# Optimization experiments

Hardware: AMD Instinct MI355X
Metric: run time of the kernel (lower is better)

Reference implementation:

```python
import jax, jax.numpy as jnp
import numpy as np

DIST = 200.0
BBOX_SP = 24
N_COARSE = 64
N_BOXES = 10
SAMPLES_ALL = N_COARSE + 2 * N_BOXES  # 84
FR_POS = 10
FR_DIR = 4
NSEM = 50
WID = 256
MERGES = [(39, 41), (27, 26), (28, 26), (29, 26), (30, 26), (31, 26), (9, 8), (35, 13)]


def posenc(x, L):
    f = 2.0 ** jnp.arange(L, dtype=x.dtype)
    xb = x[..., None, :] * f[:, None]                      # [..., L, 3]
    enc = jnp.concatenate([jnp.sin(xb), jnp.cos(xb)], -1)  # [..., L, 6]
    return jnp.concatenate([x, enc.reshape(x.shape[:-1] + (-1,))], -1)


def sample_pdf(bins, weights, n):
    # deterministic inverse-CDF sampling (det=True), bins [B,N,M], weights [B,N,M-1]
    pdf = weights / jnp.sum(weights, -1, keepdims=True)
    cdf = jnp.cumsum(pdf, -1)
    cdf = jnp.concatenate([jnp.zeros_like(cdf[..., :1]), cdf], -1)   # [B,N,M]
    B, N, M = cdf.shape
    u = jnp.linspace(0.0, 1.0, n, dtype=bins.dtype)
    cdf_f = cdf.reshape(B * N, M)
    bins_f = bins.reshape(B * N, M)
    u_f = jnp.broadcast_to(u, (B * N, n))
    inds = jax.vmap(lambda c, uu: jnp.searchsorted(c, uu, side='right'))(cdf_f, u_f)
    below = jnp.clip(inds - 1, 0, M - 1)
    above = jnp.clip(inds, 0, M - 1)
    cdf_b = jnp.take_along_axis(cdf_f, below, 1)
    cdf_a = jnp.take_along_axis(cdf_f, above, 1)
    bin_b = jnp.take_along_axis(bins_f, below, 1)
    bin_a = jnp.take_along_axis(bins_f, above, 1)
    denom = jnp.where(cdf_a - cdf_b < 1e-5, 1.0, cdf_a - cdf_b)
    t = (u_f - cdf_b) / denom
    return (bin_b + t * (bin_a - bin_b)).reshape(B, N, n)


def setup_inputs() -> dict:
    key = jax.random.key(0)
    ks = jax.random.split(key, 16)
    B, N = 1, 2048
    rays_o = jax.random.normal(ks[0], (B, N, 3)) * 2.0
    rays_d = jax.random.normal(ks[1], (B, N, 3))
    rays = jnp.concatenate([rays_o, rays_d], -1)
    near = jax.random.uniform(ks[2], (B, N, N_BOXES), minval=5.0, maxval=150.0)
    far = near + jax.random.uniform(ks[3], (B, N, N_BOXES), minval=5.0, maxval=60.0)
    inst = jax.random.randint(ks[4], (B, N, N_BOXES), 0, 20).astype(jnp.float32)
    label = jax.random.randint(ks[5], (B, N, N_BOXES), 1, NSEM).astype(jnp.float32)
    intersection = jnp.stack([near, far, inst, label], -1)  # [B,N,10,4]
    bg_noise = jax.random.uniform(ks[6], (B, N, SAMPLES_ALL))

    def lin(k, fi, fo):
        return jax.random.normal(k, (fi, fo)) / np.sqrt(fi)

    d_x = 3 + 6 * FR_POS  # 63
    d_d = 3 + 6 * FR_DIR  # 27
    params = dict(
        w_in=lin(ks[7], d_x, WID), b_in=jnp.zeros((WID,)),
        w_h=jax.random.normal(ks[8], (6, WID, WID)) / np.sqrt(WID), b_h=jnp.zeros((6, WID)),
        w_skip=lin(ks[9], WID + d_x, WID), b_skip=jnp.zeros((WID,)),
        w_sigma=lin(ks[10], WID, 1), b_sigma=jnp.zeros((1,)),
        w_feat=lin(ks[11], WID, WID), b_feat=jnp.zeros((WID,)),
        w_rgb1=lin(ks[12], WID + d_d, 128), b_rgb1=jnp.zeros((128,)),
        w_rgb2=lin(ks[13], 128, 3), b_rgb2=jnp.zeros((3,)),
        w_sem=lin(ks[14], WID, NSEM), b_sem=jnp.zeros((NSEM,)),
    )
    out = {'rays': rays, 'intersection': intersection, 'bg_noise': bg_noise}
    out.update(params)
    return out


def reference(rays, intersection, bg_noise, w_in, b_in, w_h, b_h, w_skip, b_skip,
              w_sigma, b_sigma, w_feat, b_feat, w_rgb1, b_rgb1, w_rgb2, b_rgb2,
              w_sem, b_sem):
    B, N, _ = rays.shape
    rays_o, rays_d = rays[..., :3], rays[..., 3:6]
    scale = jnp.linalg.norm(rays_d, axis=-1)  # [B,N]

    # --- ray sampling inside boxes + uniform-PDF resampling ---
    near, far = intersection[..., 0], intersection[..., 1]  # [B,N,10]
    t = jnp.linspace(0.0, 1.0, BBOX_SP)
    z_box = near[..., None] + (far - near)[..., None] * t       # [B,N,10,24]
    z_bound = jnp.concatenate([z_box[..., 0] - 1e-5, z_box[..., -1] + 1e-5], axis=2)  # [B,N,20]
    zf = jnp.sort(z_box.reshape(B, N, -1), axis=2)              # [B,N,240]
    z = sample_pdf(zf, jnp.ones_like(zf[..., 1:]), N_COARSE)    # [B,N,64]
    z = jnp.concatenate([z, z_bound], axis=2)                   # [B,N,84]
    z = jnp.where(z < 0.0, DIST + 20.0 * bg_noise, z)
    z = jnp.sort(z, axis=2)

    # --- NeRF MLP on sample points ---
    xyz = (rays_o[:, :, None] + rays_d[:, :, None] * z[..., None] / scale[..., None, None]) / DIST
    dirs = rays_d / scale[..., None]
    x_enc = posenc(xyz, FR_POS)                                 # [B,N,S,63]
    h = jax.nn.relu(x_enc @ w_in + b_in)
    for i in range(3):
        h = jax.nn.relu(h @ w_h[i] + b_h[i])
    h = jax.nn.relu(jnp.concatenate([h, x_enc], -1) @ w_skip + b_skip)
    for i in range(3, 6):
        h = jax.nn.relu(h @ w_h[i] + b_h[i])
    sigma = (h @ w_sigma + b_sigma)[..., 0]                     # [B,N,S]
    sem = h @ w_sem + b_sem                                     # [B,N,S,50]
    feat = h @ w_feat + b_feat
    d_enc = posenc(dirs, FR_DIR)                                # [B,N,27]
    d_enc = jnp.broadcast_to(d_enc[:, :, None, :], feat.shape[:-1] + (d_enc.shape[-1],))
    hr = jax.nn.relu(jnp.concatenate([feat, d_enc], -1) @ w_rgb1 + b_rgb1)
    rgb = hr @ w_rgb2 + b_rgb2                                  # [B,N,S,3]

    # --- semantic one-hot scatter + boundary masks (no-grad region) ---
    zs = jax.lax.stop_gradient(z)
    nearb = intersection[:, :, None, :, 0]                      # [B,N,1,10]
    farb = intersection[:, :, None, :, 1]
    inside = (zs[..., None] > nearb) & (zs[..., None] < farb)   # [B,N,S,10]
    d1 = zs[..., None] - farb
    d2 = nearb - zs[..., None]
    mask_bound = jnp.any(((d1 > 0) & (d1 < 1e-3)) | ((d2 > 0) & (d2 < 1e-3)), axis=-1)
    labels = intersection[..., 3].astype(jnp.int32)             # [B,N,10]
    oh_box = jax.nn.one_hot(labels, NSEM)                       # [B,N,10,50]
    one_hot = jnp.max(inside[..., None].astype(jnp.float32) * oh_box[:, :, None, :, :], axis=3)
    s0 = one_hot.sum(-1)
    mask_bbox = (zs < DIST) & (s0 == 0.0)
    mask_bg = (zs > DIST) & (s0 == 0.0)
    one_hot = one_hot.at[..., 0].set(jnp.where(mask_bbox, 1.0, one_hot[..., 0]))
    one_hot = one_hot.at[..., 23].set(jnp.where(mask_bg, 1.0, one_hot[..., 23]))
    for src, dst in MERGES:  # training-mode class merging (box/car/park/gate)
        one_hot = one_hot.at[..., dst].set(jnp.maximum(one_hot[..., dst], one_hot[..., src]))
        one_hot = one_hot.at[..., src].set(0.0)
    one_hot = jax.lax.stop_gradient(one_hot)

    # zero density outside boxes and at box boundaries
    sigma = jnp.where(mask_bbox | mask_bound, 0.0, sigma)

    # --- volumetric compositing (raw2outputs_semantic_joint) ---
    z_true = z / scale[..., None]
    dists = jnp.concatenate([z_true[..., 1:] - z_true[..., :-1],
                             jnp.full_like(z_true[..., :1], 1e10)], -1) * scale[..., None]
    alpha = 1.0 - jnp.exp(-jax.nn.relu(sigma) * dists)
    trans = jnp.cumprod(jnp.concatenate([jnp.ones_like(alpha[..., :1]),
                                         1.0 - alpha + 1e-10], -1)[..., :-1], -1)
    w = alpha * trans                                           # [B,N,S]
    rgb_map = jnp.einsum('bns,bnsc->bnc', w, jax.nn.sigmoid(rgb))
    depth = jnp.sum(w * z_true, -1)
    acc = jnp.sum(w, -1)
    sem_map = jnp.einsum('bns,bnsc->bnc', w, sem)
    return jnp.concatenate([rgb_map, depth[..., None], acc[..., None], sem_map], -1)  # [B,N,55]
```

## Files before the change

kernel.cpp:

```cpp
#include <hip/hip_runtime.h>

typedef _Float16 half8 __attribute__((ext_vector_type(8)));
typedef float f32x4 __attribute__((ext_vector_type(4)));

#define NRAYS 2048
#define SAMP 84
#define NPTS (NRAYS*SAMP)
#define SEMSTR 52

#define WT0_OFF   0
#define WTH_OFF   16384
#define WTS_OFF   409600
#define WTHD_OFF  491520
#define WTR1_OFF  573440
#define WTR2_OFF  610304
#define WT_TOTAL  612352
#define NBIAS     2512

#define OFF_WT    ((size_t)0)
#define OFF_BIAS  ((size_t)1224704)
#define OFF_Z     (OFF_BIAS + (size_t)NBIAS*4)
#define OFF_SCALE (OFF_Z + (size_t)NPTS*4)
#define OFF_SIGMA (OFF_SCALE + (size_t)NRAYS*4)
#define OFF_RGB   (OFF_SIGMA + (size_t)NPTS*4)
#define OFF_SEM   (OFF_RGB + (size_t)NPTS*12)

__global__ __launch_bounds__(256) void prep_kernel(
    const float* __restrict__ w_in,  const float* __restrict__ w_h,
    const float* __restrict__ w_skip,const float* __restrict__ w_sigma,
    const float* __restrict__ w_feat,const float* __restrict__ w_rgb1,
    const float* __restrict__ w_rgb2,const float* __restrict__ w_sem,
    const float* __restrict__ b_in,  const float* __restrict__ b_h,
    const float* __restrict__ b_skip,const float* __restrict__ b_sigma,
    const float* __restrict__ b_feat,const float* __restrict__ b_rgb1,
    const float* __restrict__ b_rgb2,const float* __restrict__ b_sem,
    _Float16* __restrict__ wt, float* __restrict__ bias)
{
  int idx = blockIdx.x*256 + threadIdx.x;
  if (idx < WT_TOTAL) {
    float v; int n, k, l, h, q;
    if (idx < WTH_OFF) {
      int r = idx; int F = r >> 10; int rem = r & 1023; int kt = rem >> 9; q = rem & 511;
      l = q >> 3; h = q & 7;
      n = F*16 + (l&15); k = kt*32 + (l>>4)*8 + h;
      v = (k < 63) ? w_in[k*256 + n] : 0.f;
    } else if (idx < WTS_OFF) {
      int r = idx - WTH_OFF; int i = r >> 16; int r2 = r & 65535;
      int F = r2 >> 12; int kt = (r2 >> 9) & 7; q = r2 & 511;
      l = q >> 3; h = q & 7;
      n = F*16 + (l&15); k = kt*32 + (l>>4)*8 + h;
      v = w_h[(i<<16) + (k<<8) + n];
    } else if (idx < WTHD_OFF) {
      int r = idx - WTS_OFF; int F = r / 5120; int rem = r % 5120; int kt = rem >> 9; q = rem & 511;
      l = q >> 3; h = q & 7;
      n = F*16 + (l&15); k = kt*32 + (l>>4)*8 + h;
      v = (k < 319) ? w_skip[k*256 + n] : 0.f;
    } else if (idx < WTR1_OFF) {
      int r = idx - WTHD_OFF; int F = r >> 12; int kt = (r >> 9) & 7; q = r & 511;
      l = q >> 3; h = q & 7;
      n = F*16 + (l&15); k = kt*32 + (l>>4)*8 + h;
      v = (n < 256) ? w_feat[(k<<8) + n]
        : (n < 306) ? w_sem[k*50 + (n-256)]
        : (n == 306)? w_sigma[k] : 0.f;
    } else if (idx < WTR2_OFF) {
      int r = idx - WTR1_OFF; int F = r / 4608; int rem = r % 4608; int kt = rem >> 9; q = rem & 511;
      l = q >> 3; h = q & 7;
      n = F*16 + (l&15); k = kt*32 + (l>>4)*8 + h;
      v = (k < 283) ? w_rgb1[k*128 + n] : 0.f;
    } else {
      int r = idx - WTR2_OFF; int kt = r >> 9; q = r & 511;
      l = q >> 3; h = q & 7;
      n = (l&15); k = kt*32 + (l>>4)*8 + h;
      v = (n < 3) ? w_rgb2[k*3 + n] : 0.f;
    }
    wt[idx] = (_Float16)v;
  } else if (idx < WT_TOTAL + NBIAS) {
    int j = idx - WT_TOTAL; float v;
    if (j < 2048) {
      int i = j >> 8, c = j & 255;
      v = (i==0) ? b_in[c] : (i<4) ? b_h[(i-1)*256+c]
        : (i==4) ? b_skip[c] : b_h[(i-2)*256+c];
    } else if (j < 2368) {
      int c = j - 2048;
      v = (c<256) ? b_feat[c] : (c<306) ? b_sem[c-256]
        : (c==306) ? b_sigma[0] : 0.f;
    } else if (j < 2496) v = b_rgb1[j-2368];
    else { int c = j-2496; v = (c<3) ? b_rgb2[c] : 0.f; }
    bias[j] = v;
  }
}

__global__ __launch_bounds__(256) void sample_kernel(
    const float* __restrict__ rays, const float* __restrict__ inter,
    const float* __restrict__ noise, float* __restrict__ zbuf,
    float* __restrict__ scaleb)
{
  __shared__ float sv[240], ss[240], z2[84];
  const int ray = blockIdx.x, t = threadIdx.x;
  const float* bx = inter + (size_t)ray*40;
  if (t < 240) {
    int b = t/24, j = t%24;
    float nr = bx[b*4], fr = bx[b*4+1];
    float tj = (j==23) ? 1.f : (float)j * (1.f/23.f);
    sv[t] = nr + (fr-nr)*tj;
  }
  __syncthreads();
  if (t < 240) {
    float v = sv[t]; int r = 0;
    for (int i = 0; i < 240; ++i) { float vi = sv[i]; r += (vi < v) || (vi == v && i < t); }
    ss[r] = v;
  }
  __syncthreads();
  if (t < 64) {
    float z;
    if (t == 63) z = ss[239];
    else { int num = t*239; int k = num/63; float f = (float)(num - k*63)*(1.f/63.f);
           z = ss[k] + f*(ss[k+1]-ss[k]); }
    z2[t] = z;
  } else if (t < 84) {
    int b = t - 64;
    z2[t] = (b < 10) ? (bx[b*4] - 1e-5f) : (bx[(b-10)*4+1] + 1e-5f);
  }
  __syncthreads();
  if (t < 84) { float z = z2[t]; if (z < 0.f) z = 200.f + 20.f*noise[(size_t)ray*84 + t]; z2[t] = z; }
  __syncthreads();
  if (t < 84) {
    float v = z2[t]; int r = 0;
    for (int i = 0; i < 84; ++i) { float vi = z2[i]; r += (vi < v) || (vi == v && i < t); }
    zbuf[(size_t)ray*84 + r] = v;
  }
  if (t == 0) {
    float dx = rays[ray*6+3], dy = rays[ray*6+4], dz = rays[ray*6+5];
    scaleb[ray] = sqrtf(dx*dx + dy*dy + dz*dz);
  }
}

#define LDS_TOTAL 81920

__device__ __forceinline__ uint32_t laddr(int m, int k) {
  return (uint32_t)(m*640) + (uint32_t)((((k>>3)^(m&7))<<4) + ((k&7)<<1));
}
struct __attribute__((aligned(8))) H4 { _Float16 h[4]; };

__device__ __forceinline__ float xenc_val(int j, float x0, float x1, float x2) {
  if (j >= 63) return 0.f;
  if (j < 3) return j==0?x0:(j==1?x1:x2);
  int q = j-3, lf = q/6, r = q%6, ci = r%3;
  float xc = (ci==0)?x0:((ci==1)?x1:x2);
  float arg = xc * (float)(1<<lf);
  return (r<3) ? sinf(arg) : cosf(arg);
}
__device__ __forceinline__ float denc_val(int c, float u0, float u1, float u2) {
  if (c >= 27) return 0.f;
  if (c < 3) return c==0?u0:(c==1?u1:u2);
  int q = c-3, lf = q/6, r = q%6, ci = r%3;
  float uc = (ci==0)?u0:((ci==1)?u1:u2);
  float arg = uc * (float)(1<<lf);
  return (r<3) ? sinf(arg) : cosf(arg);
}

template<int KT, int NF, int WN8, int MODE, bool RELU, int XOFF, bool INPLACE>
__device__ __forceinline__ void gemm(uint8_t* smem,
    const _Float16* __restrict__ WT, int fbase, const float* __restrict__ bias0,
    int p0, float* __restrict__ sigmaws, _Float16* __restrict__ semws)
{
  constexpr int MF = WN8 ? 8 : 4;
  const int t = threadIdx.x;
  const int l = t & 63, w = t >> 6;
  const int lr = l & 15, lg = l >> 4;
  const int wn = WN8 ? w : (w & 3);
  const int m0 = WN8 ? 0 : (w >> 2)*64;
  constexpr int DW   = (KT <= 3) ? KT : 4;
  constexpr int LEAD = (KT <= 3) ? KT : 3;
  f32x4 acc[NF][MF];
#pragma unroll
  for (int i = 0; i < NF; ++i)
#pragma unroll
    for (int j = 0; j < MF; ++j) acc[i][j] = (f32x4){0.f,0.f,0.f,0.f};
  const _Float16* wb = WT + (size_t)((fbase + wn*NF)*KT)*512 + (size_t)l*8;
  half8 av[DW][NF];
  half8 bv[2][MF];
  auto baddr = [&](int mf, int kt)->uint32_t {
    return laddr(m0 + mf*16 + lr, XOFF + kt*32 + lg*8);
  };
#pragma unroll
  for (int d = 0; d < LEAD && d < KT; ++d)
#pragma unroll
    for (int nf = 0; nf < NF; ++nf)
      av[d][nf] = *(const half8*)(wb + (size_t)(nf*KT + d)*512);
#pragma unroll
  for (int mf = 0; mf < MF; ++mf)
    bv[0][mf] = *(const half8*)(smem + baddr(mf, 0));
#pragma unroll
  for (int kt = 0; kt < KT; ++kt) {
    if (kt + 1 < KT) {
#pragma unroll
      for (int mf = 0; mf < MF; ++mf)
        bv[(kt+1)&1][mf] = *(const half8*)(smem + baddr(mf, kt+1));
    }
    if (kt + LEAD < KT) {
#pragma unroll
      for (int nf = 0; nf < NF; ++nf)
        av[(kt+LEAD)%DW][nf] = *(const half8*)(wb + (size_t)(nf*KT + kt + LEAD)*512);
    }
    __builtin_amdgcn_sched_barrier(0);
#pragma unroll
    for (int nf = 0; nf < NF; ++nf)
#pragma unroll
      for (int mf = 0; mf < MF; ++mf)
        acc[nf][mf] = __builtin_amdgcn_mfma_f32_16x16x32_f16(av[kt%DW][nf], bv[kt&1][mf], acc[nf][mf], 0, 0, 0);
    __builtin_amdgcn_sched_barrier(0);
  }
  if (INPLACE) __syncthreads();
#pragma unroll
  for (int nf = 0; nf < NF; ++nf) {
    const int n0 = (fbase + wn*NF + nf)*16;
    const int nb = n0 + lg*4;
    const f32x4 bvv = *(const f32x4*)(bias0 + nb);
    if (MODE == 0 || n0 < 256) {
#pragma unroll
      for (int mf = 0; mf < MF; ++mf) {
        const int m = m0 + mf*16 + lr;
        f32x4 v = acc[nf][mf] + bvv;
        H4 hh;
#pragma unroll
        for (int r = 0; r < 4; ++r) { float x = v[r]; if (RELU) x = fmaxf(x, 0.f); hh.h[r] = (_Float16)x; }
        *(H4*)(smem + laddr(m, nb)) = hh;
      }
    } else {
      const int cb = nb - 256;
#pragma unroll
      for (int mf = 0; mf < MF; ++mf) {
        const int m = m0 + mf*16 + lr;
        const int pp = p0 + m;
        f32x4 v = acc[nf][mf] + bvv;
        if (cb <= 44) {
          H4 hh;
#pragma unroll
          for (int r = 0; r < 4; ++r) hh.h[r] = (_Float16)v[r];
          *(H4*)(semws + (size_t)pp*SEMSTR + cb) = hh;
        } else if (cb == 48) {
          semws[(size_t)pp*SEMSTR + 48] = (_Float16)v[0];
          semws[(size_t)pp*SEMSTR + 49] = (_Float16)v[1];
          sigmaws[pp] = v[2];
        }
      }
    }
  }
}

__device__ __forceinline__ void gemm_rgb2(uint8_t* smem,
    const _Float16* __restrict__ WT, const float* __restrict__ bias,
    int p0, float* __restrict__ rgbws)
{
  const int t = threadIdx.x;
  const int l = t & 63, w = t >> 6;
  const int lr = l & 15, lg = l >> 4;
  const int m0 = w*16;
  f32x4 acc = (f32x4){0.f,0.f,0.f,0.f};
#pragma unroll
  for (int kt = 0; kt < 4; ++kt) {
    half8 a = *(const half8*)(WT + (size_t)kt*512 + (size_t)l*8);
    half8 b = *(const half8*)(smem + laddr(m0 + lr, kt*32 + lg*8));
    acc = __builtin_amdgcn_mfma_f32_16x16x32_f16(a, b, acc, 0, 0, 0);
  }
  const int pp = p0 + m0 + lr;
#pragma unroll
  for (int r = 0; r < 4; ++r) {
    const int n = lg*4 + r;
    if (n < 3) rgbws[(size_t)pp*3 + n] = (float)acc[r] + bias[n];
  }
}

__global__ __launch_bounds__(512,2) void mlp_kernel(
    const float* __restrict__ rays, const float* __restrict__ zbuf,
    const float* __restrict__ scaleb, const _Float16* __restrict__ wt,
    const float* __restrict__ bias, float* __restrict__ sigmaws,
    float* __restrict__ rgbws, _Float16* __restrict__ semws)
{
  extern __shared__ uint8_t smem[];
  const int p0 = blockIdx.x*128;
  const int t = threadIdx.x;
  const int m = t & 127, g = t >> 7;
  const int p = p0 + m;
  const int ray = p / SAMP;
  const float sc = scaleb[ray];
  const float z  = zbuf[p];
  const float ox = rays[ray*6+0], oy = rays[ray*6+1], oz = rays[ray*6+2];
  const float dx = rays[ray*6+3], dy = rays[ray*6+4], dz = rays[ray*6+5];
  const float x0 = (ox + dx*z/sc)/200.f;
  const float x1 = (oy + dy*z/sc)/200.f;
  const float x2 = (oz + dz*z/sc)/200.f;
  const float u0 = dx/sc, u1 = dy/sc, u2 = dz/sc;
  {
    union { _Float16 hv[8]; half8 v; } u8;
#pragma unroll
    for (int hf = 0; hf < 2; ++hf) {
      const int j0 = g*16 + hf*8;
#pragma unroll
      for (int jj = 0; jj < 8; ++jj) u8.hv[jj] = (_Float16)xenc_val(j0+jj, x0, x1, x2);
      *(half8*)(smem + laddr(m, 256 + j0)) = u8.v;
    }
  }
  __syncthreads();
  gemm<2 ,2,1,0,true ,256,false>(smem, wt+WT0_OFF,         0,  bias+0,    p0, sigmaws, semws); __syncthreads();
  gemm<8 ,2,1,0,true ,0  ,true >(smem, wt+WTH_OFF+0*65536, 0,  bias+256,  p0, sigmaws, semws); __syncthreads();
  gemm<8 ,2,1,0,true ,0  ,true >(smem, wt+WTH_OFF+1*65536, 0,  bias+512,  p0, sigmaws, semws); __syncthreads();
  gemm<8 ,2,1,0,true ,0  ,true >(smem, wt+WTH_OFF+2*65536, 0,  bias+768,  p0, sigmaws, semws); __syncthreads();
  gemm<10,2,1,0,true ,0  ,true >(smem, wt+WTS_OFF,         0,  bias+1024, p0, sigmaws, semws); __syncthreads();
  {
    union { _Float16 hv[8]; half8 v; } u8;
    const int c0 = g*8;
#pragma unroll
    for (int cc = 0; cc < 8; ++cc) u8.hv[cc] = (_Float16)denc_val(c0+cc, u0, u1, u2);
    *(half8*)(smem + laddr(m, 256 + c0)) = u8.v;
  }
  gemm<8 ,2,1,0,true ,0  ,true >(smem, wt+WTH_OFF+3*65536, 0,  bias+1280, p0, sigmaws, semws); __syncthreads();
  gemm<8 ,2,1,0,true ,0  ,true >(smem, wt+WTH_OFF+4*65536, 0,  bias+1536, p0, sigmaws, semws); __syncthreads();
  gemm<8 ,2,1,0,true ,0  ,true >(smem, wt+WTH_OFF+5*65536, 0,  bias+1792, p0, sigmaws, semws); __syncthreads();
  gemm<8 ,1,0,1,false,0  ,false>(smem, wt+WTHD_OFF,        16, bias+2048, p0, sigmaws, semws);
  gemm<8 ,2,1,0,false,0  ,true >(smem, wt+WTHD_OFF,        0,  bias+2048, p0, sigmaws, semws); __syncthreads();
  gemm<9 ,1,1,0,true ,0  ,true >(smem, wt+WTR1_OFF,        0,  bias+2368, p0, sigmaws, semws); __syncthreads();
  gemm_rgb2(smem, wt+WTR2_OFF, bias+2496, p0, rgbws);
}

__global__ __launch_bounds__(128) void comp_kernel(
    const float* __restrict__ inter, const float* __restrict__ zbuf,
    const float* __restrict__ scaleb, const float* __restrict__ sigmaws,
    const float* __restrict__ rgbws, const _Float16* __restrict__ semws,
    float* __restrict__ out)
{
  __shared__ float zt[84], alpha[84], wgt[84];
  const int ray = blockIdx.x, t = threadIdx.x;
  const float sc = scaleb[ray];
  const float* bx = inter + (size_t)ray*40;
  if (t < 84) zt[t] = zbuf[(size_t)ray*84 + t] / sc;
  __syncthreads();
  if (t < 84) {
    const float z = zbuf[(size_t)ray*84 + t];
    bool inside = false, bound = false;
    for (int b = 0; b < 10; ++b) {
      const float nr = bx[b*4], fr = bx[b*4+1];
      inside = inside || (z > nr && z < fr);
      const float d1 = z - fr, d2 = nr - z;
      bound = bound || (d1 > 0.f && d1 < 1e-3f) || (d2 > 0.f && d2 < 1e-3f);
    }
    float sg = sigmaws[(size_t)ray*84 + t];
    const bool bbox = (z < 200.f) && !inside;
    if (bbox || bound) sg = 0.f;
    sg = fmaxf(sg, 0.f);
    const float dist = (t < 83) ? (zt[t+1] - zt[t])*sc : 1e10f*sc;
    alpha[t] = 1.f - expf(-sg*dist);
  }
  __syncthreads();
  if (t == 0) {
    float T = 1.f;
    for (int s = 0; s < 84; ++s) { wgt[s] = alpha[s]*T; T *= (1.f - alpha[s] + 1e-10f); }
  }
  __syncthreads();
  if (t < 55) {
    float a = 0.f;
    const size_t base = (size_t)ray*84;
    if (t < 50) {
      for (int s = 0; s < 84; ++s) a += wgt[s]*(float)semws[(base+s)*SEMSTR + t];
      out[(size_t)ray*55 + 5 + t] = a;
    } else if (t < 53) {
      const int c = t - 50;
      for (int s = 0; s < 84; ++s) { const float r = rgbws[(base+s)*3 + c]; a += wgt[s]/(1.f + expf(-r)); }
      out[(size_t)ray*55 + c] = a;
    } else if (t == 53) {
      for (int s = 0; s < 84; ++s) a += wgt[s]*zt[s];
      out[(size_t)ray*55 + 3] = a;
    } else {
      for (int s = 0; s < 84; ++s) a += wgt[s];
      out[(size_t)ray*55 + 4] = a;
    }
  }
}

extern "C" void kernel_launch(void* const* d_in, const int* in_sizes, int n_in,
                              void* d_out, int out_size, void* d_ws, size_t ws_size,
                              hipStream_t stream) {
  const float* rays   = (const float*)d_in[0];
  const float* inter  = (const float*)d_in[1];
  const float* noise  = (const float*)d_in[2];
  const float* w_in   = (const float*)d_in[3];
  const float* b_in   = (const float*)d_in[4];
  const float* w_h    = (const float*)d_in[5];
  const float* b_h    = (const float*)d_in[6];
  const float* w_skip = (const float*)d_in[7];
  const float* b_skip = (const float*)d_in[8];
  const float* w_sig  = (const float*)d_in[9];
  const float* b_sig  = (const float*)d_in[10];
  const float* w_feat = (const float*)d_in[11];
  const float* b_feat = (const float*)d_in[12];
  const float* w_rgb1 = (const float*)d_in[13];
  const float* b_rgb1 = (const float*)d_in[14];
  const float* w_rgb2 = (const float*)d_in[15];
  const float* b_rgb2 = (const float*)d_in[16];
  const float* w_sem  = (const float*)d_in[17];
  const float* b_sem  = (const float*)d_in[18];

  uint8_t* ws = (uint8_t*)d_ws;
  _Float16* wt    = (_Float16*)(ws + OFF_WT);
  float* bias     = (float*)(ws + OFF_BIAS);
  float* zbuf     = (float*)(ws + OFF_Z);
  float* scaleb   = (float*)(ws + OFF_SCALE);
  float* sigmaws  = (float*)(ws + OFF_SIGMA);
  float* rgbws    = (float*)(ws + OFF_RGB);
  _Float16* semws = (_Float16*)(ws + OFF_SEM);

  prep_kernel<<<dim3((WT_TOTAL + NBIAS + 255)/256), dim3(256), 0, stream>>>(
      w_in, w_h, w_skip, w_sig, w_feat, w_rgb1, w_rgb2, w_sem,
      b_in, b_h, b_skip, b_sig, b_feat, b_rgb1, b_rgb2, b_sem, wt, bias);
  sample_kernel<<<dim3(NRAYS), dim3(256), 0, stream>>>(rays, inter, noise, zbuf, scaleb);
  mlp_kernel<<<dim3(NPTS/128), dim3(512), LDS_TOTAL, stream>>>(
      rays, zbuf, scaleb, wt, bias, sigmaws, rgbws, semws);
  comp_kernel<<<dim3(NRAYS), dim3(128), 0, stream>>>(
      inter, zbuf, scaleb, sigmaws, rgbws, semws, (float*)d_out);
}
```

Baseline: 286.4 us.

## Switch MLP GEMMs to 32x32x16 MFMA with 64-point blocks of 256 threads

Repacks all weight tiles for the 32x32x16 f16 MFMA instruction and rewrites the GEMM helper and its epilogue to use 16-element accumulators. The MLP kernel now processes 64 points per block with 4 waves and half the LDS, with occupancy raised to 3 blocks. The goal is fewer MFMA issues and less LDS operand traffic per FLOP, plus more resident blocks for latency hiding. In exchange each block reuses weights over fewer points, so more weight loads go to global or L2, and one sync after the skip layer was moved.

```diff
diff --git a/kernel.cpp b/kernel.cpp
--- a/kernel.cpp
+++ b/kernel.cpp
@@ -1,7 +1,8 @@
 #include <hip/hip_runtime.h>
 
 typedef _Float16 half8 __attribute__((ext_vector_type(8)));
-typedef float f32x4 __attribute__((ext_vector_type(4)));
+typedef float f32x4  __attribute__((ext_vector_type(4)));
+typedef float f32x16 __attribute__((ext_vector_type(16)));
 
 #define NRAYS 2048
 #define SAMP 84
@@ -14,11 +15,11 @@
 #define WTHD_OFF  491520
 #define WTR1_OFF  573440
 #define WTR2_OFF  610304
-#define WT_TOTAL  612352
+#define WT_TOTAL  614400
 #define NBIAS     2512
 
 #define OFF_WT    ((size_t)0)
-#define OFF_BIAS  ((size_t)1224704)
+#define OFF_BIAS  ((size_t)1228800)
 #define OFF_Z     (OFF_BIAS + (size_t)NBIAS*4)
 #define OFF_SCALE (OFF_Z + (size_t)NPTS*4)
 #define OFF_SIGMA (OFF_SCALE + (size_t)NRAYS*4)
@@ -38,39 +39,43 @@
 {
   int idx = blockIdx.x*256 + threadIdx.x;
   if (idx < WT_TOTAL) {
-    float v; int n, k, l, h, q;
+    float v; int n, k, l, h, kt, F, rem;
     if (idx < WTH_OFF) {
-      int r = idx; int F = r >> 10; int rem = r & 1023; int kt = rem >> 9; q = rem & 511;
-      l = q >> 3; h = q & 7;
-      n = F*16 + (l&15); k = kt*32 + (l>>4)*8 + h;
+      F = idx >> 11; rem = idx & 2047; kt = rem >> 9; int q = rem & 511;
+      l = q >> 3; h = q & 7;
+      n = F*32 + (l&31); k = kt*16 + ((l>>5)<<3) + h;
       v = (k < 63) ? w_in[k*256 + n] : 0.f;
     } else if (idx < WTS_OFF) {
-      int r = idx - WTH_OFF; int i = r >> 16; int r2 = r & 65535;
-      int F = r2 >> 12; int kt = (r2 >> 9) & 7; q = r2 & 511;
-      l = q >> 3; h = q & 7;
-      n = F*16 + (l&15); k = kt*32 + (l>>4)*8 + h;
+      int r = idx - WTH_OFF; int i = r >> 16; int rr = r & 65535;
+      F = rr >> 13; rem = rr & 8191; kt = rem >> 9; int q = rem & 511;
+      l = q >> 3; h = q & 7;
+      n = F*32 + (l&31); k = kt*16 + ((l>>5)<<3) + h;
       v = w_h[(i<<16) + (k<<8) + n];
     } else if (idx < WTHD_OFF) {
-      int r = idx - WTS_OFF; int F = r / 5120; int rem = r % 5120; int kt = rem >> 9; q = rem & 511;
-      l = q >> 3; h = q & 7;
-      n = F*16 + (l&15); k = kt*32 + (l>>4)*8 + h;
+      int r = idx - WTS_OFF;
+      F = r / 10240; rem = r % 10240; kt = rem >> 9; int q = rem & 511;
+      l = q >> 3; h = q & 7;
+      n = F*32 + (l&31); k = kt*16 + ((l>>5)<<3) + h;
       v = (k < 319) ? w_skip[k*256 + n] : 0.f;
     } else if (idx < WTR1_OFF) {
-      int r = idx - WTHD_OFF; int F = r >> 12; int kt = (r >> 9) & 7; q = r & 511;
-      l = q >> 3; h = q & 7;
-      n = F*16 + (l&15); k = kt*32 + (l>>4)*8 + h;
+      int r = idx - WTHD_OFF;
+      F = r >> 13; rem = r & 8191; kt = rem >> 9; int q = rem & 511;
+      l = q >> 3; h = q & 7;
+      n = F*32 + (l&31); k = kt*16 + ((l>>5)<<3) + h;
       v = (n < 256) ? w_feat[(k<<8) + n]
         : (n < 306) ? w_sem[k*50 + (n-256)]
         : (n == 306)? w_sigma[k] : 0.f;
     } else if (idx < WTR2_OFF) {
-      int r = idx - WTR1_OFF; int F = r / 4608; int rem = r % 4608; int kt = rem >> 9; q = rem & 511;
-      l = q >> 3; h = q & 7;
-      n = F*16 + (l&15); k = kt*32 + (l>>4)*8 + h;
+      int r = idx - WTR1_OFF;
+      F = r / 9216; rem = r % 9216; kt = rem >> 9; int q = rem & 511;
+      l = q >> 3; h = q & 7;
+      n = F*32 + (l&31); k = kt*16 + ((l>>5)<<3) + h;
       v = (k < 283) ? w_rgb1[k*128 + n] : 0.f;
     } else {
-      int r = idx - WTR2_OFF; int kt = r >> 9; q = r & 511;
-      l = q >> 3; h = q & 7;
-      n = (l&15); k = kt*32 + (l>>4)*8 + h;
+      int r = idx - WTR2_OFF;
+      kt = r >> 9; int q = r & 511;
+      l = q >> 3; h = q & 7;
+      n = (l&31); k = kt*16 + ((l>>5)<<3) + h;
       v = (n < 3) ? w_rgb2[k*3 + n] : 0.f;
     }
     wt[idx] = (_Float16)v;
@@ -135,7 +140,7 @@
   }
 }
 
-#define LDS_TOTAL 81920
+#define LDS_TOTAL 40960
 
 __device__ __forceinline__ uint32_t laddr(int m, int k) {
   return (uint32_t)(m*640) + (uint32_t)((((k>>3)^(m&7))<<4) + ((k&7)<<1));
@@ -159,29 +164,29 @@
   return (r<3) ? sinf(arg) : cosf(arg);
 }
 
-template<int KT, int NF, int WN8, int MODE, bool RELU, int XOFF, bool INPLACE>
+template<int KT, int NF, int MODE, bool RELU, int XOFF, bool INPLACE>
 __device__ __forceinline__ void gemm(uint8_t* smem,
     const _Float16* __restrict__ WT, int fbase, const float* __restrict__ bias0,
     int p0, float* __restrict__ sigmaws, _Float16* __restrict__ semws)
 {
-  constexpr int MF = WN8 ? 8 : 4;
+  constexpr int MF = 2;
   const int t = threadIdx.x;
-  const int l = t & 63, w = t >> 6;
-  const int lr = l & 15, lg = l >> 4;
-  const int wn = WN8 ? w : (w & 3);
-  const int m0 = WN8 ? 0 : (w >> 2)*64;
+  const int l = t & 63, wn = t >> 6;
+  const int lr = l & 31, lg = l >> 5;
   constexpr int DW   = (KT <= 3) ? KT : 4;
   constexpr int LEAD = (KT <= 3) ? KT : 3;
-  f32x4 acc[NF][MF];
+  f32x16 acc[NF][MF];
 #pragma unroll
   for (int i = 0; i < NF; ++i)
 #pragma unroll
-    for (int j = 0; j < MF; ++j) acc[i][j] = (f32x4){0.f,0.f,0.f,0.f};
+    for (int j = 0; j < MF; ++j)
+#pragma unroll
+      for (int r = 0; r < 16; ++r) acc[i][j][r] = 0.f;
   const _Float16* wb = WT + (size_t)((fbase + wn*NF)*KT)*512 + (size_t)l*8;
   half8 av[DW][NF];
   half8 bv[2][MF];
   auto baddr = [&](int mf, int kt)->uint32_t {
-    return laddr(m0 + mf*16 + lr, XOFF + kt*32 + lg*8);
+    return laddr(mf*32 + lr, XOFF + kt*16 + lg*8);
   };
 #pragma unroll
   for (int d = 0; d < LEAD && d < KT; ++d)
@@ -208,41 +213,42 @@
     for (int nf = 0; nf < NF; ++nf)
 #pragma unroll
       for (int mf = 0; mf < MF; ++mf)
-        acc[nf][mf] = __builtin_amdgcn_mfma_f32_16x16x32_f16(av[kt%DW][nf], bv[kt&1][mf], acc[nf][mf], 0, 0, 0);
+        acc[nf][mf] = __builtin_amdgcn_mfma_f32_32x32x16_f16(
+            av[kt%DW][nf], bv[kt&1][mf], acc[nf][mf], 0, 0, 0);
     __builtin_amdgcn_sched_barrier(0);
   }
   if (INPLACE) __syncthreads();
 #pragma unroll
   for (int nf = 0; nf < NF; ++nf) {
-    const int n0 = (fbase + wn*NF + nf)*16;
-    const int nb = n0 + lg*4;
-    const f32x4 bvv = *(const f32x4*)(bias0 + nb);
-    if (MODE == 0 || n0 < 256) {
-#pragma unroll
-      for (int mf = 0; mf < MF; ++mf) {
-        const int m = m0 + mf*16 + lr;
-        f32x4 v = acc[nf][mf] + bvv;
-        H4 hh;
-#pragma unroll
-        for (int r = 0; r < 4; ++r) { float x = v[r]; if (RELU) x = fmaxf(x, 0.f); hh.h[r] = (_Float16)x; }
-        *(H4*)(smem + laddr(m, nb)) = hh;
-      }
-    } else {
-      const int cb = nb - 256;
-#pragma unroll
-      for (int mf = 0; mf < MF; ++mf) {
-        const int m = m0 + mf*16 + lr;
-        const int pp = p0 + m;
-        f32x4 v = acc[nf][mf] + bvv;
-        if (cb <= 44) {
-          H4 hh;
-#pragma unroll
-          for (int r = 0; r < 4; ++r) hh.h[r] = (_Float16)v[r];
-          *(H4*)(semws + (size_t)pp*SEMSTR + cb) = hh;
-        } else if (cb == 48) {
-          semws[(size_t)pp*SEMSTR + 48] = (_Float16)v[0];
-          semws[(size_t)pp*SEMSTR + 49] = (_Float16)v[1];
-          sigmaws[pp] = v[2];
+    const int ncol0 = (fbase + wn*NF + nf)*32;
+#pragma unroll
+    for (int mf = 0; mf < MF; ++mf) {
+      const int m = mf*32 + lr;
+      const f32x16 v = acc[nf][mf];
+#pragma unroll
+      for (int g = 0; g < 4; ++g) {
+        const int nst = ncol0 + 8*g + 4*lg;
+        const f32x4 b4 = *(const f32x4*)(bias0 + nst);
+        float x0 = v[4*g+0] + b4[0], x1 = v[4*g+1] + b4[1];
+        float x2 = v[4*g+2] + b4[2], x3 = v[4*g+3] + b4[3];
+        if (RELU) { x0 = fmaxf(x0,0.f); x1 = fmaxf(x1,0.f);
+                    x2 = fmaxf(x2,0.f); x3 = fmaxf(x3,0.f); }
+        if (MODE == 0) {
+          H4 hh; hh.h[0]=(_Float16)x0; hh.h[1]=(_Float16)x1;
+                 hh.h[2]=(_Float16)x2; hh.h[3]=(_Float16)x3;
+          *(H4*)(smem + laddr(m, nst)) = hh;
+        } else {
+          const int cb = nst - 256;
+          const int pp = p0 + m;
+          if (cb <= 44) {
+            H4 hh; hh.h[0]=(_Float16)x0; hh.h[1]=(_Float16)x1;
+                   hh.h[2]=(_Float16)x2; hh.h[3]=(_Float16)x3;
+            *(H4*)(semws + (size_t)pp*SEMSTR + cb) = hh;
+          } else if (cb == 48) {
+            semws[(size_t)pp*SEMSTR + 48] = (_Float16)x0;
+            semws[(size_t)pp*SEMSTR + 49] = (_Float16)x1;
+            sigmaws[pp] = x2;
+          }
         }
       }
     }
@@ -255,33 +261,36 @@
 {
   const int t = threadIdx.x;
   const int l = t & 63, w = t >> 6;
-  const int lr = l & 15, lg = l >> 4;
-  const int m0 = w*16;
-  f32x4 acc = (f32x4){0.f,0.f,0.f,0.f};
-#pragma unroll
-  for (int kt = 0; kt < 4; ++kt) {
-    half8 a = *(const half8*)(WT + (size_t)kt*512 + (size_t)l*8);
-    half8 b = *(const half8*)(smem + laddr(m0 + lr, kt*32 + lg*8));
-    acc = __builtin_amdgcn_mfma_f32_16x16x32_f16(a, b, acc, 0, 0, 0);
-  }
-  const int pp = p0 + m0 + lr;
-#pragma unroll
-  for (int r = 0; r < 4; ++r) {
-    const int n = lg*4 + r;
-    if (n < 3) rgbws[(size_t)pp*3 + n] = (float)acc[r] + bias[n];
-  }
-}
-
-__global__ __launch_bounds__(512,2) void mlp_kernel(
+  if (w >= 2) return;
+  const int lr = l & 31, lg = l >> 5;
+  f32x16 acc;
+#pragma unroll
+  for (int r = 0; r < 16; ++r) acc[r] = 0.f;
+  const _Float16* wb = WT + (size_t)l*8;
+#pragma unroll
+  for (int kt = 0; kt < 8; ++kt) {
+    half8 a = *(const half8*)(wb + (size_t)kt*512);
+    half8 b = *(const half8*)(smem + laddr(w*32 + lr, kt*16 + lg*8));
+    acc = __builtin_amdgcn_mfma_f32_32x32x16_f16(a, b, acc, 0, 0, 0);
+  }
+  if (lg == 0) {
+    const int pp = p0 + w*32 + lr;
+#pragma unroll
+    for (int r = 0; r < 3; ++r)
+      rgbws[(size_t)pp*3 + r] = acc[r] + bias[r];
+  }
+}
+
+__global__ __launch_bounds__(256,3) void mlp_kernel(
     const float* __restrict__ rays, const float* __restrict__ zbuf,
     const float* __restrict__ scaleb, const _Float16* __restrict__ wt,
     const float* __restrict__ bias, float* __restrict__ sigmaws,
     float* __restrict__ rgbws, _Float16* __restrict__ semws)
 {
   extern __shared__ uint8_t smem[];
-  const int p0 = blockIdx.x*128;
+  const int p0 = blockIdx.x*64;
   const int t = threadIdx.x;
-  const int m = t & 127, g = t >> 7;
+  const int m = t & 63, g = t >> 6;
   const int p = p0 + m;
   const int ray = p / SAMP;
   const float sc = scaleb[ray];
@@ -303,11 +312,11 @@
     }
   }
   __syncthreads();
-  gemm<2 ,2,1,0,true ,256,false>(smem, wt+WT0_OFF,         0,  bias+0,    p0, sigmaws, semws); __syncthreads();
-  gemm<8 ,2,1,0,true ,0  ,true >(smem, wt+WTH_OFF+0*65536, 0,  bias+256,  p0, sigmaws, semws); __syncthreads();
-  gemm<8 ,2,1,0,true ,0  ,true >(smem, wt+WTH_OFF+1*65536, 0,  bias+512,  p0, sigmaws, semws); __syncthreads();
-  gemm<8 ,2,1,0,true ,0  ,true >(smem, wt+WTH_OFF+2*65536, 0,  bias+768,  p0, sigmaws, semws); __syncthreads();
-  gemm<10,2,1,0,true ,0  ,true >(smem, wt+WTS_OFF,         0,  bias+1024, p0, sigmaws, semws); __syncthreads();
+  gemm<4 ,2,0,true ,256,false>(smem, wt+WT0_OFF,         0, bias+0,    p0, sigmaws, semws); __syncthreads();
+  gemm<16,2,0,true ,0  ,true >(smem, wt+WTH_OFF+0*65536, 0, bias+256,  p0, sigmaws, semws); __syncthreads();
+  gemm<16,2,0,true ,0  ,true >(smem, wt+WTH_OFF+1*65536, 0, bias+512,  p0, sigmaws, semws); __syncthreads();
+  gemm<16,2,0,true ,0  ,true >(smem, wt+WTH_OFF+2*65536, 0, bias+768,  p0, sigmaws, semws); __syncthreads();
+  gemm<20,2,0,true ,0  ,true >(smem, wt+WTS_OFF,         0, bias+1024, p0, sigmaws, semws);
   {
     union { _Float16 hv[8]; half8 v; } u8;
     const int c0 = g*8;
@@ -315,12 +324,14 @@
     for (int cc = 0; cc < 8; ++cc) u8.hv[cc] = (_Float16)denc_val(c0+cc, u0, u1, u2);
     *(half8*)(smem + laddr(m, 256 + c0)) = u8.v;
   }
-  gemm<8 ,2,1,0,true ,0  ,true >(smem, wt+WTH_OFF+3*65536, 0,  bias+1280, p0, sigmaws, semws); __syncthreads();
-  gemm<8 ,2,1,0,true ,0  ,true >(smem, wt+WTH_OFF+4*65536, 0,  bias+1536, p0, sigmaws, semws); __syncthreads();
-  gemm<8 ,2,1,0,true ,0  ,true >(smem, wt+WTH_OFF+5*65536, 0,  bias+1792, p0, sigmaws, semws); __syncthreads();
-  gemm<8 ,1,0,1,false,0  ,false>(smem, wt+WTHD_OFF,        16, bias+2048, p0, sigmaws, semws);
-  gemm<8 ,2,1,0,false,0  ,true >(smem, wt+WTHD_OFF,        0,  bias+2048, p0, sigmaws, semws); __syncthreads();
-  gemm<9 ,1,1,0,true ,0  ,true >(smem, wt+WTR1_OFF,        0,  bias+2368, p0, sigmaws, semws); __syncthreads();
+  __syncthreads();
+  gemm<16,2,0,true ,0  ,true >(smem, wt+WTH_OFF+3*65536, 0, bias+1280, p0, sigmaws, semws); __syncthreads();
+  gemm<16,2,0,true ,0  ,true >(smem, wt+WTH_OFF+4*65536, 0, bias+1536, p0, sigmaws, semws); __syncthreads();
+  gemm<16,2,0,true ,0  ,true >(smem, wt+WTH_OFF+5*65536, 0, bias+1792, p0, sigmaws, semws); __syncthreads();
+  if ((t >> 6) < 2)
+    gemm<16,1,1,false,0 ,false>(smem, wt+WTHD_OFF,        8, bias+2048, p0, sigmaws, semws);
+  gemm<16,2,0,false,0  ,true >(smem, wt+WTHD_OFF,        0, bias+2048, p0, sigmaws, semws); __syncthreads();
+  gemm<18,1,0,true ,0  ,true >(smem, wt+WTR1_OFF,        0, bias+2368, p0, sigmaws, semws); __syncthreads();
   gemm_rgb2(smem, wt+WTR2_OFF, bias+2496, p0, rgbws);
 }
 
@@ -414,7 +425,7 @@
       w_in, w_h, w_skip, w_sig, w_feat, w_rgb1, w_rgb2, w_sem,
       b_in, b_h, b_skip, b_sig, b_feat, b_rgb1, b_rgb2, b_sem, wt, bias);
   sample_kernel<<<dim3(NRAYS), dim3(256), 0, stream>>>(rays, inter, noise, zbuf, scaleb);
-  mlp_kernel<<<dim3(NPTS/128), dim3(512), LDS_TOTAL, stream>>>(
+  mlp_kernel<<<dim3(NPTS/64), dim3(256), LDS_TOTAL, stream>>>(
       rays, zbuf, scaleb, wt, bias, sigmaws, rgbws, semws);
   comp_kernel<<<dim3(NRAYS), dim3(128), 0, stream>>>(
       inter, zbuf, scaleb, sigmaws, rgbws, semws, (float*)d_out);
```

After: 292.6 us. 2.2% more time.
